# Kernel optimization log

Measured on AMD Instinct MI355X. Metric: run time of the kernel, lower is better.

The kernel has to match this reference:

```python
import jax, jax.numpy as jnp
import numpy as np

B, N = 256, 20000

def setup_inputs() -> dict:
    key = jax.random.key(0)
    k1, k2 = jax.random.split(key)
    x_in = jax.random.normal(k1, (B, 1, N, 4), dtype=jnp.float32)
    weights = jax.random.uniform(k2, (B, N), dtype=jnp.float32)
    return {"x_in": x_in, "weights": weights}

def reference(x_in, weights):
    # weighted_8points: x_in [B,1,N,4] -> e_hat [B,9]
    b, _, n, _ = x_in.shape
    xx = x_in[:, 0, :, :]                      # [B,N,4] = (x1, y1, x2, y2)
    x1, y1, x2, y2 = xx[..., 0], xx[..., 1], xx[..., 2], xx[..., 3]
    ones = jnp.ones_like(x1)
    # Epipolar design matrix rows: [x2*x1, x2*y1, x2, y2*x1, y2*y1, y2, x1, y1, 1]
    X = jnp.stack([x2 * x1, x2 * y1, x2,
                   y2 * x1, y2 * y1, y2,
                   x1, y1, ones], axis=-1)      # [B,N,9]
    wX = weights[:, :, None] * X                # [B,N,9]
    XwX = jnp.einsum('bni,bnj->bij', X, wX)     # [B,9,9] symmetric
    # batch_symeig: eigenvectors ascending by eigenvalue; smallest -> column 0
    _, v = jnp.linalg.eigh(XwX)                 # [B,9,9]
    e_hat = v[:, :, 0]                          # [B,9]
    e_hat = e_hat / jnp.linalg.norm(e_hat, axis=1, keepdims=True)
    return e_hat
```

## Files before the change

### kernel.cpp

```cpp
#include <hip/hip_runtime.h>
#include <math.h>

#define BATCH 256
#define NPTS  20000
#define NCHUNK 4
#define PERCH (NPTS / NCHUNK)

__global__ __launch_bounds__(256) void gram_kernel(
    const float4* __restrict__ x, const float* __restrict__ w,
    double* __restrict__ partial)
{
    int b = blockIdx.x;
    int chunk = blockIdx.y;
    int tid = threadIdx.x;

    float acc[45];
#pragma unroll
    for (int k = 0; k < 45; ++k) acc[k] = 0.0f;

    const float4* xb = x + (size_t)b * NPTS;
    const float*  wb = w + (size_t)b * NPTS;
    int base = chunk * PERCH;
    for (int n = base + tid; n < base + PERCH; n += 256) {
        float4 v = xb[n];
        float wt = wb[n];
        float X[9];
        X[0] = v.z * v.x; X[1] = v.z * v.y; X[2] = v.z;
        X[3] = v.w * v.x; X[4] = v.w * v.y; X[5] = v.w;
        X[6] = v.x;       X[7] = v.y;       X[8] = 1.0f;
        int idx = 0;
#pragma unroll
        for (int j = 0; j < 9; ++j) {
            float wXj = wt * X[j];
#pragma unroll
            for (int i = j; i < 9; ++i) {
                acc[idx] += X[i] * wXj;
                ++idx;
            }
        }
    }

#pragma unroll
    for (int k = 0; k < 45; ++k) {
        float v = acc[k];
        for (int off = 32; off > 0; off >>= 1)
            v += __shfl_down(v, off, 64);
        acc[k] = v;
    }
    __shared__ float red[4][45];
    int lane = tid & 63, wv = tid >> 6;
    if (lane == 0) {
#pragma unroll
        for (int k = 0; k < 45; ++k) red[wv][k] = acc[k];
    }
    __syncthreads();
    if (tid < 45) {
        double s = (double)red[0][tid] + (double)red[1][tid]
                 + (double)red[2][tid] + (double)red[3][tid];
        partial[((size_t)b * NCHUNK + chunk) * 45 + tid] = s;
    }
}


__device__ __forceinline__ float f_sign(float a, float b) {
    return (b >= 0.0f) ? fabsf(a) : -fabsf(a);
}

__device__ __forceinline__ float slapy2(float xx, float yy) {
    float xa = fabsf(xx), ya = fabsf(yy);
    float w_ = fmaxf(xa, ya), z_ = fminf(xa, ya);
    if (z_ == 0.0f) return w_;
    float t = z_ / w_;
    return w_ * sqrtf(1.0f + t * t);
}

__device__ __forceinline__ float rdl(float v, int i) {
    return __int_as_float(__builtin_amdgcn_readlane(__float_as_int(v), i));
}

__device__ __forceinline__ void slartg(float f, float g, float* cs, float* sn, float* r) {
    if (g == 0.0f) { *cs = 1.0f; *sn = 0.0f; *r = f; }
    else if (f == 0.0f) { *cs = 0.0f; *sn = (g >= 0.0f) ? 1.0f : -1.0f; *r = fabsf(g); }
    else {
        float dd2 = sqrtf(f * f + g * g);
        *cs = fabsf(f) / dd2;
        *r  = f_sign(dd2, f);
        *sn = g / (*r);
    }
}

__device__ void slaev2(float a, float b, float c_, float* rt1, float* rt2,
                       float* cs1, float* sn1) {
    float sm = a + c_;
    float df = a - c_;
    float adf = fabsf(df);
    float tb = b + b;
    float ab = fabsf(tb);
    float acmx, acmn;
    if (fabsf(a) > fabsf(c_)) { acmx = a; acmn = c_; } else { acmx = c_; acmn = a; }
    float rt;
    if (adf > ab)      { float t = ab / adf; rt = adf * sqrtf(1.0f + t * t); }
    else if (adf < ab) { float t = adf / ab; rt = ab * sqrtf(1.0f + t * t); }
    else               { rt = ab * sqrtf(2.0f); }
    int sgn1;
    if (sm < 0.0f) {
        *rt1 = 0.5f * (sm - rt); sgn1 = -1;
        *rt2 = (acmx / (*rt1)) * acmn - (b / (*rt1)) * b;
    } else if (sm > 0.0f) {
        *rt1 = 0.5f * (sm + rt); sgn1 = 1;
        *rt2 = (acmx / (*rt1)) * acmn - (b / (*rt1)) * b;
    } else {
        *rt1 = 0.5f * rt; *rt2 = -0.5f * rt; sgn1 = 1;
    }
    float cs; int sgn2;
    if (df >= 0.0f) { cs = df + rt; sgn2 = 1; } else { cs = df - rt; sgn2 = -1; }
    float acs = fabsf(cs);
    if (acs > ab) {
        float ct = -tb / cs;
        *sn1 = 1.0f / sqrtf(1.0f + ct * ct);
        *cs1 = ct * (*sn1);
    } else {
        if (ab == 0.0f) { *cs1 = 1.0f; *sn1 = 0.0f; }
        else {
            float tn = -cs / tb;
            *cs1 = 1.0f / sqrtf(1.0f + tn * tn);
            *sn1 = tn * (*cs1);
        }
    }
    if (sgn1 == sgn2) { float tn = *cs1; *cs1 = -(*sn1); *sn1 = tn; }
}

#define APPLY_QL() do { \
    _Pragma("unroll") \
    for (int jz = 8; jz >= 1; --jz) { \
        float cj = rdl(r_cw, jz), sj = rdl(r_sw, jz); \
        float tmpz = zz[jz + 1]; \
        zz[jz + 1] = cj * tmpz - sj * zz[jz]; \
        zz[jz]     = sj * tmpz + cj * zz[jz]; \
    } } while (0)

#define APPLY_QR() do { \
    _Pragma("unroll") \
    for (int jz = 1; jz <= 8; ++jz) { \
        float cj = rdl(r_cw, jz), sj = rdl(r_sw, jz); \
        float tmpz = zz[jz + 1]; \
        zz[jz + 1] = cj * tmpz - sj * zz[jz]; \
        zz[jz]     = sj * tmpz + cj * zz[jz]; \
    } } while (0)

__global__ __launch_bounds__(64) void eig_kernel(
    const double* __restrict__ partial, float* __restrict__ out)
{
    const int n = 9;
    int b = blockIdx.x;
    int lane = threadIdx.x;

    __shared__ float A[10][10];
    __shared__ float Zl[10][10];
    __shared__ float ddl[11], eel[11], tau[10], wv[10], zv[10];

    float zz[10];
    float r_dd, r_ee, r_cw, r_sw;

    if (lane < 45) {
        const double* p = partial + (size_t)b * (45 * NCHUNK) + lane;
        double s = ((p[0] + p[45]) + p[90]) + p[135];
        int idx = lane, j = 1;
        while (idx >= 10 - j) { idx -= (10 - j); ++j; }
        int i = j + idx;
        A[i][j] = (float)s;
    }

    for (int i = 1; i <= n - 1; ++i) {
        float alpha = A[i + 1][i];
        float ssq = 0.0f;
        for (int k = i + 2; k <= n; ++k) ssq += A[k][i] * A[k][i];
        float xnorm = sqrtf(ssq);
        float taui;
        if (xnorm == 0.0f) {
            taui = 0.0f;
            if (lane == 0) eel[i] = alpha;
        } else {
            float beta = -f_sign(slapy2(alpha, xnorm), alpha);
            taui = (beta - alpha) / beta;
            float sc = 1.0f / (alpha - beta);
            if (lane < 8 - i) {
                int k = i + 2 + lane;
                A[k][i] *= sc;
            }
            if (lane == 0) eel[i] = beta;
        }
        if (taui != 0.0f) {
            if (lane < 9 - i) {
                int r2 = i + 1 + lane;
                float s2 = 0.0f;
                for (int c2 = i + 1; c2 <= n; ++c2) {
                    float aval = (r2 >= c2) ? A[r2][c2] : A[c2][r2];
                    float vc = (c2 == i + 1) ? 1.0f : A[c2][i];
                    s2 += aval * vc;
                }
                wv[r2] = taui * s2;
            }
            float dot = 0.0f;
            for (int k = i + 1; k <= n; ++k) {
                float vk = (k == i + 1) ? 1.0f : A[k][i];
                dot += wv[k] * vk;
            }
            float alpha2 = -0.5f * taui * dot;
            if (lane < 9 - i) {
                int k = i + 1 + lane;
                float vk = (k == i + 1) ? 1.0f : A[k][i];
                wv[k] += alpha2 * vk;
            }
            int kk = 9 - i;
            int cnt = kk * (kk + 1) / 2;
            if (lane < cnt) {
                int idx = lane, cc = 0;
                while (idx >= kk - cc) { idx -= (kk - cc); ++cc; }
                int c2 = i + 1 + cc;
                int r2 = c2 + idx;
                float vr = (r2 == i + 1) ? 1.0f : A[r2][i];
                float vc = (c2 == i + 1) ? 1.0f : A[c2][i];
                A[r2][c2] -= vr * wv[c2] + wv[r2] * vc;
            }
        }
        if (lane == 0) { ddl[i] = A[i][i]; tau[i] = taui; }
    }
    if (lane == 0) ddl[n] = A[n][n];

    r_dd = 0.0f; r_ee = 0.0f;
    if (lane >= 1 && lane <= 9) r_dd = ddl[lane];
    if (lane >= 1 && lane <= 8) r_ee = eel[lane];

#pragma unroll
    for (int c0 = 1; c0 <= 9; ++c0) zz[c0] = (lane == c0) ? 1.0f : 0.0f;

    const float eps    = 5.9604645e-8f;
    const float eps2   = eps * eps;
    const float safmin = 1.17549435e-38f;
    const float safmax = 1.0f / 1.17549435e-38f;
    const float ssfmax = sqrtf(safmax) / 3.0f;
    const float ssfmin = sqrtf(safmin) / eps2;

    int nmaxit = n * 30, jtot = 0;
    int l1 = 1, nm1 = n - 1;
    int l, m, lsv, lend, lendsv, iscale;
    float anorm, p, g, r, c, s, f, btmp, rt1, rt2, tst, mul;

L10:
    if (l1 > n) goto L160;
    if (l1 > 1) r_ee = (lane == l1 - 1) ? 0.0f : r_ee;
    if (l1 <= nm1) {
        for (m = l1; m <= nm1; ++m) {
            tst = fabsf(rdl(r_ee, m));
            if (tst == 0.0f) goto L30;
            if (tst <= (sqrtf(fabsf(rdl(r_dd, m))) * sqrtf(fabsf(rdl(r_dd, m + 1)))) * eps) {
                r_ee = (lane == m) ? 0.0f : r_ee;
                goto L30;
            }
        }
    }
    m = n;
L30:
    l = l1; lsv = l; lend = m; lendsv = lend; l1 = m + 1;
    if (lend == l) goto L10;

    anorm = 0.0f;
    for (int k = l; k <= lend; ++k) anorm = fmaxf(anorm, fabsf(rdl(r_dd, k)));
    for (int k = l; k <= lend - 1; ++k) anorm = fmaxf(anorm, fabsf(rdl(r_ee, k)));
    iscale = 0;
    if (anorm == 0.0f) goto L10;
    if (anorm > ssfmax) {
        iscale = 1; mul = ssfmax / anorm;
        r_dd = (lane >= l && lane <= lend)     ? r_dd * mul : r_dd;
        r_ee = (lane >= l && lane <= lend - 1) ? r_ee * mul : r_ee;
    } else if (anorm < ssfmin) {
        iscale = 2; mul = ssfmin / anorm;
        r_dd = (lane >= l && lane <= lend)     ? r_dd * mul : r_dd;
        r_ee = (lane >= l && lane <= lend - 1) ? r_ee * mul : r_ee;
    }

    if (fabsf(rdl(r_dd, lend)) < fabsf(rdl(r_dd, l))) { lend = lsv; l = lendsv; }

    if (lend > l) {
L40:
        if (l != lend) {
            for (m = l; m <= lend - 1; ++m) {
                tst = fabsf(rdl(r_ee, m)); tst = tst * tst;
                if (tst <= (eps2 * fabsf(rdl(r_dd, m))) * fabsf(rdl(r_dd, m + 1)) + safmin) goto L60;
            }
        }
        m = lend;
L60:
        if (m < lend) r_ee = (lane == m) ? 0.0f : r_ee;
        p = rdl(r_dd, l);
        if (m == l) goto L80;
        if (m == l + 1) {
            slaev2(rdl(r_dd, l), rdl(r_ee, l), rdl(r_dd, l + 1), &rt1, &rt2, &c, &s);
            r_cw = 1.0f; r_sw = 0.0f;
            r_cw = (lane == l) ? c : r_cw;
            r_sw = (lane == l) ? s : r_sw;
            APPLY_QL();
            r_dd = (lane == l) ? rt1 : ((lane == l + 1) ? rt2 : r_dd);
            r_ee = (lane == l) ? 0.0f : r_ee;
            l += 2;
            if (l <= lend) goto L40;
            goto L140;
        }
        if (jtot == nmaxit) goto L140;
        ++jtot;
        g = (rdl(r_dd, l + 1) - p) / (2.0f * rdl(r_ee, l));
        r = slapy2(g, 1.0f);
        g = rdl(r_dd, m) - p + rdl(r_ee, l) / (g + f_sign(r, g));
        s = 1.0f; c = 1.0f; p = 0.0f;
        r_cw = 1.0f; r_sw = 0.0f;
        for (int i = m - 1; i >= l; --i) {
            float ei = rdl(r_ee, i);
            f = s * ei; btmp = c * ei;
            slartg(g, f, &c, &s, &r);
            if (i != m - 1) r_ee = (lane == i + 1) ? r : r_ee;
            g = rdl(r_dd, i + 1) - p;
            r = (rdl(r_dd, i) - g) * s + 2.0f * c * btmp;
            p = s * r;
            r_dd = (lane == i + 1) ? (g + p) : r_dd;
            g = c * r - btmp;
            r_cw = (lane == i) ? c : r_cw;
            r_sw = (lane == i) ? (-s) : r_sw;
        }
        APPLY_QL();
        r_dd = (lane == l) ? (r_dd - p) : r_dd;
        r_ee = (lane == l) ? g : r_ee;
        goto L40;
L80:
        r_dd = (lane == l) ? p : r_dd;
        l = l + 1;
        if (l <= lend) goto L40;
        goto L140;
    } else {
L90:
        if (l != lend) {
            for (m = l; m >= lend + 1; --m) {
                tst = fabsf(rdl(r_ee, m - 1)); tst = tst * tst;
                if (tst <= (eps2 * fabsf(rdl(r_dd, m))) * fabsf(rdl(r_dd, m - 1)) + safmin) goto L110;
            }
        }
        m = lend;
L110:
        if (m > lend) r_ee = (lane == m - 1) ? 0.0f : r_ee;
        p = rdl(r_dd, l);
        if (m == l) goto L130;
        if (m == l - 1) {
            slaev2(rdl(r_dd, l - 1), rdl(r_ee, l - 1), rdl(r_dd, l), &rt1, &rt2, &c, &s);
            r_cw = 1.0f; r_sw = 0.0f;
            r_cw = (lane == l - 1) ? c : r_cw;
            r_sw = (lane == l - 1) ? s : r_sw;
            APPLY_QR();
            r_dd = (lane == l - 1) ? rt1 : ((lane == l) ? rt2 : r_dd);
            r_ee = (lane == l - 1) ? 0.0f : r_ee;
            l -= 2;
            if (l >= lend) goto L90;
            goto L140;
        }
        if (jtot == nmaxit) goto L140;
        ++jtot;
        g = (rdl(r_dd, l - 1) - p) / (2.0f * rdl(r_ee, l - 1));
        r = slapy2(g, 1.0f);
        g = rdl(r_dd, m) - p + rdl(r_ee, l - 1) / (g + f_sign(r, g));
        s = 1.0f; c = 1.0f; p = 0.0f;
        r_cw = 1.0f; r_sw = 0.0f;
        for (int i = m; i <= l - 1; ++i) {
            float ei = rdl(r_ee, i);
            f = s * ei; btmp = c * ei;
            slartg(g, f, &c, &s, &r);
            if (i != m) r_ee = (lane == i - 1) ? r : r_ee;
            g = rdl(r_dd, i) - p;
            r = (rdl(r_dd, i + 1) - g) * s + 2.0f * c * btmp;
            p = s * r;
            r_dd = (lane == i) ? (g + p) : r_dd;
            g = c * r - btmp;
            r_cw = (lane == i) ? c : r_cw;
            r_sw = (lane == i) ? s : r_sw;
        }
        APPLY_QR();
        r_dd = (lane == l) ? (r_dd - p) : r_dd;
        r_ee = (lane == l - 1) ? g : r_ee;
        goto L90;
L130:
        r_dd = (lane == l) ? p : r_dd;
        l = l - 1;
        if (l >= lend) goto L90;
        goto L140;
    }

L140:
    if (iscale == 1) {
        mul = anorm / ssfmax;
        r_dd = (lane >= lsv && lane <= lendsv)     ? r_dd * mul : r_dd;
        r_ee = (lane >= lsv && lane <= lendsv - 1) ? r_ee * mul : r_ee;
    } else if (iscale == 2) {
        mul = anorm / ssfmin;
        r_dd = (lane >= lsv && lane <= lendsv)     ? r_dd * mul : r_dd;
        r_ee = (lane >= lsv && lane <= lendsv - 1) ? r_ee * mul : r_ee;
    }
    if (jtot < nmaxit) goto L10;
    goto L160;

L160:
    if (lane >= 1 && lane <= 9) {
#pragma unroll
        for (int c0 = 1; c0 <= 9; ++c0) Zl[lane][c0] = zz[c0];
    }

    for (int ii = 2; ii <= n; ++ii) {
        int i = ii - 1, k = i;
        p = rdl(r_dd, i);
        for (int j = ii; j <= n; ++j) {
            float dj = rdl(r_dd, j);
            if (dj < p) { k = j; p = dj; }
        }
        if (k != i) {
            float di = rdl(r_dd, i);
            r_dd = (lane == k) ? di : r_dd;
            r_dd = (lane == i) ? p  : r_dd;
            if (lane >= 1 && lane <= 9) {
                float t = Zl[lane][i]; Zl[lane][i] = Zl[lane][k]; Zl[lane][k] = t;
            }
        }
    }

    if (lane < 9) zv[lane + 1] = Zl[lane + 1][1];
    for (int i2 = n - 1; i2 >= 1; --i2) {
        float ti = tau[i2];
        if (ti != 0.0f) {
            float dotp = zv[i2 + 1];
            for (int k = i2 + 2; k <= n; ++k) dotp += A[k][i2] * zv[k];
            float t = ti * dotp;
            if (lane < 9 - i2) {
                int k = i2 + 1 + lane;
                float upd = (k == i2 + 1) ? t : t * A[k][i2];
                zv[k] -= upd;
            }
        }
    }
    {
        float nrm = 0.0f;
        for (int row = 1; row <= n; ++row) nrm += zv[row] * zv[row];
        nrm = sqrtf(nrm);
        if (lane < 9) out[(size_t)b * 9 + lane] = zv[lane + 1] / nrm;
    }
}

extern "C" void kernel_launch(void* const* d_in, const int* in_sizes, int n_in,
                              void* d_out, int out_size, void* d_ws, size_t ws_size,
                              hipStream_t stream) {
    const float4* x = (const float4*)d_in[0];
    const float*  w = (const float*)d_in[1];
    float* out = (float*)d_out;
    double* partial = (double*)d_ws;

    gram_kernel<<<dim3(BATCH, NCHUNK), dim3(256), 0, stream>>>(x, w, partial);
    eig_kernel<<<dim3(BATCH), dim3(64), 0, stream>>>(partial, out);
}
```

Before: 193.2 us.

## Fuse Gram accumulation and eigen solve into one kernel per batch

Merges the Gram-matrix reduction kernel and the eigensolver kernel into a single 512-thread kernel per batch element. Each of the 8 waves handles two of the 16 chunk/wave slices, writes its reduced partials to shared memory, and the first wave then sums them in double and runs the eigensolver. This removes the second launch and the global-memory round trip for the partials. The cost is fewer blocks (256 instead of 1024) in the bandwidth-bound reduction phase, and 7 of 8 waves sitting idle during the serial eigen phase.

New measurement: 193.5 us. No clear change (+0.1%).

```diff
diff --git a/kernel.cpp b/kernel.cpp
--- a/kernel.cpp
+++ b/kernel.cpp
@@ -3,63 +3,6 @@
 
 #define BATCH 256
 #define NPTS  20000
-#define NCHUNK 4
-#define PERCH (NPTS / NCHUNK)
-
-__global__ __launch_bounds__(256) void gram_kernel(
-    const float4* __restrict__ x, const float* __restrict__ w,
-    double* __restrict__ partial)
-{
-    int b = blockIdx.x;
-    int chunk = blockIdx.y;
-    int tid = threadIdx.x;
-
-    float acc[45];
-#pragma unroll
-    for (int k = 0; k < 45; ++k) acc[k] = 0.0f;
-
-    const float4* xb = x + (size_t)b * NPTS;
-    const float*  wb = w + (size_t)b * NPTS;
-    int base = chunk * PERCH;
-    for (int n = base + tid; n < base + PERCH; n += 256) {
-        float4 v = xb[n];
-        float wt = wb[n];
-        float X[9];
-        X[0] = v.z * v.x; X[1] = v.z * v.y; X[2] = v.z;
-        X[3] = v.w * v.x; X[4] = v.w * v.y; X[5] = v.w;
-        X[6] = v.x;       X[7] = v.y;       X[8] = 1.0f;
-        int idx = 0;
-#pragma unroll
-        for (int j = 0; j < 9; ++j) {
-            float wXj = wt * X[j];
-#pragma unroll
-            for (int i = j; i < 9; ++i) {
-                acc[idx] += X[i] * wXj;
-                ++idx;
-            }
-        }
-    }
-
-#pragma unroll
-    for (int k = 0; k < 45; ++k) {
-        float v = acc[k];
-        for (int off = 32; off > 0; off >>= 1)
-            v += __shfl_down(v, off, 64);
-        acc[k] = v;
-    }
-    __shared__ float red[4][45];
-    int lane = tid & 63, wv = tid >> 6;
-    if (lane == 0) {
-#pragma unroll
-        for (int k = 0; k < 45; ++k) red[wv][k] = acc[k];
-    }
-    __syncthreads();
-    if (tid < 45) {
-        double s = (double)red[0][tid] + (double)red[1][tid]
-                 + (double)red[2][tid] + (double)red[3][tid];
-        partial[((size_t)b * NCHUNK + chunk) * 45 + tid] = s;
-    }
-}
 
 
 __device__ __forceinline__ float f_sign(float a, float b) {
@@ -148,23 +91,74 @@
         zz[jz]     = sj * tmpz + cj * zz[jz]; \
     } } while (0)
 
-__global__ __launch_bounds__(64) void eig_kernel(
-    const double* __restrict__ partial, float* __restrict__ out)
+__global__ __launch_bounds__(512) void fused_kernel(
+    const float4* __restrict__ x, const float* __restrict__ wgt,
+    float* __restrict__ out)
 {
     const int n = 9;
     int b = blockIdx.x;
-    int lane = threadIdx.x;
-
+    int tid = threadIdx.x;
+    int lane = tid & 63;
+    int rw = tid >> 6;
+
+    __shared__ float red[16][45];
     __shared__ float A[10][10];
     __shared__ float Zl[10][10];
-    __shared__ float ddl[11], eel[11], tau[10], wv[10], zv[10];
-
-    float zz[10];
-    float r_dd, r_ee, r_cw, r_sw;
+    __shared__ float ddl[11], eel[11], tau[10], wvl[10], zvl[10];
+
+    for (int half = 0; half < 2; ++half) {
+        int v = rw * 2 + half;
+        int chunk = v >> 2, wvc = v & 3;
+        float acc[45];
+#pragma unroll
+        for (int k = 0; k < 45; ++k) acc[k] = 0.0f;
+
+        const float4* xb = x + (size_t)b * NPTS;
+        const float*  wb = wgt + (size_t)b * NPTS;
+        int base = chunk * 5000;
+        for (int nn = base + wvc * 64 + lane; nn < base + 5000; nn += 256) {
+            float4 vv = xb[nn];
+            float wt = wb[nn];
+            float X[9];
+            X[0] = vv.z * vv.x; X[1] = vv.z * vv.y; X[2] = vv.z;
+            X[3] = vv.w * vv.x; X[4] = vv.w * vv.y; X[5] = vv.w;
+            X[6] = vv.x;        X[7] = vv.y;        X[8] = 1.0f;
+            int idx = 0;
+#pragma unroll
+            for (int j = 0; j < 9; ++j) {
+                float wXj = wt * X[j];
+#pragma unroll
+                for (int i = j; i < 9; ++i) {
+                    acc[idx] += X[i] * wXj;
+                    ++idx;
+                }
+            }
+        }
+#pragma unroll
+        for (int k = 0; k < 45; ++k) {
+            float vred = acc[k];
+            for (int off = 32; off > 0; off >>= 1)
+                vred += __shfl_down(vred, off, 64);
+            acc[k] = vred;
+        }
+        if (lane == 0) {
+#pragma unroll
+            for (int k = 0; k < 45; ++k) red[v][k] = acc[k];
+        }
+    }
+    __syncthreads();
+    if (tid >= 64) return;
 
     if (lane < 45) {
-        const double* p = partial + (size_t)b * (45 * NCHUNK) + lane;
-        double s = ((p[0] + p[45]) + p[90]) + p[135];
+        double p0 = (double)red[0][lane]  + (double)red[1][lane]
+                  + (double)red[2][lane]  + (double)red[3][lane];
+        double p1 = (double)red[4][lane]  + (double)red[5][lane]
+                  + (double)red[6][lane]  + (double)red[7][lane];
+        double p2 = (double)red[8][lane]  + (double)red[9][lane]
+                  + (double)red[10][lane] + (double)red[11][lane];
+        double p3 = (double)red[12][lane] + (double)red[13][lane]
+                  + (double)red[14][lane] + (double)red[15][lane];
+        double s = ((p0 + p1) + p2) + p3;
         int idx = lane, j = 1;
         while (idx >= 10 - j) { idx -= (10 - j); ++j; }
         int i = j + idx;
@@ -199,18 +193,18 @@
                     float vc = (c2 == i + 1) ? 1.0f : A[c2][i];
                     s2 += aval * vc;
                 }
-                wv[r2] = taui * s2;
+                wvl[r2] = taui * s2;
             }
             float dot = 0.0f;
             for (int k = i + 1; k <= n; ++k) {
                 float vk = (k == i + 1) ? 1.0f : A[k][i];
-                dot += wv[k] * vk;
+                dot += wvl[k] * vk;
             }
             float alpha2 = -0.5f * taui * dot;
             if (lane < 9 - i) {
                 int k = i + 1 + lane;
                 float vk = (k == i + 1) ? 1.0f : A[k][i];
-                wv[k] += alpha2 * vk;
+                wvl[k] += alpha2 * vk;
             }
             int kk = 9 - i;
             int cnt = kk * (kk + 1) / 2;
@@ -221,17 +215,18 @@
                 int r2 = c2 + idx;
                 float vr = (r2 == i + 1) ? 1.0f : A[r2][i];
                 float vc = (c2 == i + 1) ? 1.0f : A[c2][i];
-                A[r2][c2] -= vr * wv[c2] + wv[r2] * vc;
+                A[r2][c2] -= vr * wvl[c2] + wvl[r2] * vc;
             }
         }
         if (lane == 0) { ddl[i] = A[i][i]; tau[i] = taui; }
     }
     if (lane == 0) ddl[n] = A[n][n];
 
+    float r_dd, r_ee, r_cw, r_sw;
+    float zz[10];
     r_dd = 0.0f; r_ee = 0.0f;
     if (lane >= 1 && lane <= 9) r_dd = ddl[lane];
     if (lane >= 1 && lane <= 8) r_ee = eel[lane];
-
 #pragma unroll
     for (int c0 = 1; c0 <= 9; ++c0) zz[c0] = (lane == c0) ? 1.0f : 0.0f;
 
@@ -428,25 +423,25 @@
         }
     }
 
-    if (lane < 9) zv[lane + 1] = Zl[lane + 1][1];
+    if (lane < 9) zvl[lane + 1] = Zl[lane + 1][1];
     for (int i2 = n - 1; i2 >= 1; --i2) {
         float ti = tau[i2];
         if (ti != 0.0f) {
-            float dotp = zv[i2 + 1];
-            for (int k = i2 + 2; k <= n; ++k) dotp += A[k][i2] * zv[k];
+            float dotp = zvl[i2 + 1];
+            for (int k = i2 + 2; k <= n; ++k) dotp += A[k][i2] * zvl[k];
             float t = ti * dotp;
             if (lane < 9 - i2) {
                 int k = i2 + 1 + lane;
                 float upd = (k == i2 + 1) ? t : t * A[k][i2];
-                zv[k] -= upd;
+                zvl[k] -= upd;
             }
         }
     }
     {
         float nrm = 0.0f;
-        for (int row = 1; row <= n; ++row) nrm += zv[row] * zv[row];
+        for (int row = 1; row <= n; ++row) nrm += zvl[row] * zvl[row];
         nrm = sqrtf(nrm);
-        if (lane < 9) out[(size_t)b * 9 + lane] = zv[lane + 1] / nrm;
+        if (lane < 9) out[(size_t)b * 9 + lane] = zvl[lane + 1] / nrm;
     }
 }
 
@@ -456,8 +451,7 @@
     const float4* x = (const float4*)d_in[0];
     const float*  w = (const float*)d_in[1];
     float* out = (float*)d_out;
-    double* partial = (double*)d_ws;
-
-    gram_kernel<<<dim3(BATCH, NCHUNK), dim3(256), 0, stream>>>(x, w, partial);
-    eig_kernel<<<dim3(BATCH), dim3(64), 0, stream>>>(partial, out);
-}
+    (void)d_ws; (void)ws_size;
+
+    fused_kernel<<<dim3(BATCH), dim3(512), 0, stream>>>(x, w, out);
+}
```
